# Optimization experiments

Hardware: AMD Instinct MI355X
Metric: run time of the kernel (lower is better)

Reference implementation:

```python
import jax, jax.numpy as jnp
import numpy as np

B, AT, NBR = 8, 96, 512
NG, NT = 25, 5            # n_gaussian_triple, n_theta
NANG = NG * NT            # 125, filternet input dim
NF = 128                  # n_filters
NB = 128                  # n_atom_basis


def ssp(x):
    # shifted softplus: ln(0.5*e^x + 0.5) = softplus(x) - ln(2)
    return jax.nn.softplus(x) - jnp.asarray(np.log(2.0), x.dtype)


def setup_inputs() -> dict:
    key = jax.random.key(0)
    ks = jax.random.split(key, 16)
    s = lambda fan_in: 1.0 / np.sqrt(fan_in)
    return {
        "x": jax.random.normal(ks[0], (B, AT, NB), jnp.float32),
        "triple_ijk": jax.random.uniform(ks[1], (B, AT, NBR, NANG), jnp.float32),
        "neighbors_j": jax.random.randint(ks[2], (B, AT, NBR), 0, AT, jnp.int32),
        "neighbors_k": jax.random.randint(ks[3], (B, AT, NBR), 0, AT, jnp.int32),
        "triple_mask": jnp.ones((B, AT, NBR), jnp.float32),
        # filter network (Dense ssp -> Dense linear)
        "W1": jax.random.normal(ks[4], (NANG, NF), jnp.float32) * s(NANG),
        "b1": jnp.zeros((NF,), jnp.float32),
        "W2": jax.random.normal(ks[5], (NF, NF), jnp.float32) * s(NF),
        "b2": jnp.zeros((NF,), jnp.float32),
        # cfconv in2f (no bias) and f2out (ssp activation)
        "Win": jax.random.normal(ks[6], (NB, NF), jnp.float32) * s(NB),
        "Wf2": jax.random.normal(ks[7], (NF, NB), jnp.float32) * s(NF),
        "bf2": jnp.zeros((NB,), jnp.float32),
        # final dense (linear) before residual
        "Wd": jax.random.normal(ks[8], (NB, NB), jnp.float32) * s(NB),
        "bd": jnp.zeros((NB,), jnp.float32),
    }


def _gather_atoms(y, nbh):
    # y: (B, At, F); nbh: (B, At, Nbr) -> (B, At, Nbr, F)
    b, at, nbr = nbh.shape
    idx = nbh.reshape(b, at * nbr, 1)
    return jnp.take_along_axis(y, idx, axis=1).reshape(b, at, nbr, y.shape[-1])


def reference(x, triple_ijk, neighbors_j, neighbors_k, triple_mask,
              W1, b1, W2, b2, Win, Wf2, bf2, Wd, bd):
    # filter network on angular/radial triple features -> (B, At, Nbr, NF)
    W_triple = ssp(triple_ijk @ W1 + b1) @ W2 + b2
    # in2f
    y = x @ Win                                  # (B, At, NF)
    y_j = _gather_atoms(y, neighbors_j)          # (B, At, Nbr, NF)
    y_k = _gather_atoms(y, neighbors_k)          # (B, At, Nbr, NF)
    # element-wise continuous-filter conv over triples, mask padded triples
    yt = y_j * y_k * W_triple * triple_mask[..., None]
    agg = jnp.sum(yt, axis=2)                    # sum-aggregate over triples
    v = ssp(agg @ Wf2 + bf2)                     # f2out with shifted softplus
    v = v @ Wd + bd                              # interaction dense
    return x + v                                 # residual
```

## Files before the change

### kernel.cpp

```cpp
#include <hip/hip_runtime.h>
#include <math.h>

#define B_    8
#define AT_   96
#define NBR_  512
#define NANG_ 125
#define NF_   128
#define NB_   128
#define TN    32
#define NCHUNK 8
#define CROWS (NBR_ / NCHUNK)
#define TSTRIDE 136

typedef __attribute__((ext_vector_type(8))) short bf16x8;
typedef __attribute__((ext_vector_type(4))) float f32x4;
typedef float f32x4u __attribute__((ext_vector_type(4), aligned(4)));
typedef __attribute__((ext_vector_type(4))) unsigned int u32x4;

__device__ __forceinline__ short f2bf(float f) {
    union { float f; unsigned u; } x; x.f = f;
    return (short)((x.u + 0x8000u) >> 16);
}
__device__ __forceinline__ float bf2f(unsigned short h) {
    union { unsigned u; float f; } x; x.u = ((unsigned)h) << 16;
    return x.f;
}
__device__ __forceinline__ unsigned pk2bf(float a, float b) {
    union { float f; unsigned u; } x, y; x.f = a; y.f = b;
    return ((x.u + 0x8000u) >> 16) | ((y.u + 0x8000u) & 0xffff0000u);
}

__device__ __forceinline__ float sspf(float x) {
    float p = __builtin_amdgcn_exp2f(x * 1.44269504088896340736f);
    float l = __builtin_amdgcn_logf(1.0f + p);
    return 0.69314718055994530942f * l - 0.69314718055994530942f;
}

__global__ __launch_bounds__(128) void prep_kernel(
    const float* __restrict__ x, const float* __restrict__ Win,
    const float* __restrict__ W1, const float* __restrict__ W2,
    float* __restrict__ y, short* __restrict__ w1p, short* __restrict__ w2p)
{
    __shared__ float xs[4][NB_];
    int blk = blockIdx.x, tid = threadIdx.x;
    if (blk < 192) {
        int row0 = blk * 4;
        #pragma unroll
        for (int r = 0; r < 4; r++) xs[r][tid] = x[(row0 + r) * NB_ + tid];
        __syncthreads();
        float a0 = 0.f, a1 = 0.f, a2 = 0.f, a3 = 0.f;
        #pragma unroll 8
        for (int k = 0; k < NB_; k++) {
            float w = Win[k * NF_ + tid];
            a0 = fmaf(xs[0][k], w, a0);
            a1 = fmaf(xs[1][k], w, a1);
            a2 = fmaf(xs[2][k], w, a2);
            a3 = fmaf(xs[3][k], w, a3);
        }
        y[(row0 + 0) * NF_ + tid] = a0;
        y[(row0 + 1) * NF_ + tid] = a1;
        y[(row0 + 2) * NF_ + tid] = a2;
        y[(row0 + 3) * NF_ + tid] = a3;
    } else {
        int t = (blk - 192) * 128 + tid;
        int j = t & 7, lane = (t >> 3) & 63, ks = (t >> 9) & 3, ct = t >> 11;
        int k = ks * 32 + (lane >> 4) * 8 + j;
        int n = ct * 16 + (lane & 15);
        w1p[t] = (k < NANG_) ? f2bf(W1[k * NF_ + n]) : (short)0;
        w2p[t] = f2bf(W2[k * NF_ + n]);
    }
}

__global__ __launch_bounds__(256) void triple_partial(
    const float* __restrict__ trip,
    const int* __restrict__ nbj, const int* __restrict__ nbk,
    const float* __restrict__ maskg,
    const float* __restrict__ b1g, const float* __restrict__ b2g,
    const float* __restrict__ y, const short* __restrict__ w1p,
    const short* __restrict__ w2p, float* __restrict__ pagg)
{
    __shared__ short ts[TN * TSTRIDE];
    __shared__ short hs[TN * TSTRIDE];
    __shared__ unsigned short yjkb[TN * TSTRIDE];

    const int tid = threadIdx.x;
    const int wave = tid >> 6, lane = tid & 63;
    const int quad = lane >> 4, col = lane & 15;
    const int blk = blockIdx.x;
    const int bid = blk >> 3, c = blk & 7;
    const int b = bid / AT_;

    const float* tpc = trip + (long)bid * NBR_ * NANG_ + (long)c * CROWS * NANG_;
    const int nb_base = bid * NBR_ + c * CROWS;

    const int ct0 = 2 * wave, ct1 = 2 * wave + 1;
    const int f0 = ct0 * 16 + col, f1 = ct1 * 16 + col;
    const float bias1_0 = b1g[f0], bias1_1 = b1g[f1];
    const float bias2_0 = b2g[f0], bias2_1 = b2g[f1];

    const int srow = tid >> 3, schunk = tid & 7;

    bf16x8 w1f0[4], w1f1[4], w2f0[4], w2f1[4];
    #pragma unroll
    for (int ks = 0; ks < 4; ks++) {
        w1f0[ks] = *(const bf16x8*)&w1p[(ct0 * 4 + ks) * 512 + lane * 8];
        w1f1[ks] = *(const bf16x8*)&w1p[(ct1 * 4 + ks) * 512 + lane * 8];
        w2f0[ks] = *(const bf16x8*)&w2p[(ct0 * 4 + ks) * 512 + lane * 8];
        w2f1[ks] = *(const bf16x8*)&w2p[(ct1 * 4 + ks) * 512 + lane * 8];
    }

    float accw0 = 0.f, accw1 = 0.f;

    for (int nt = 0; nt < CROWS / TN; nt++) {
        const float* tp = tpc + nt * TN * NANG_;
        const int nrow0 = nb_base + nt * TN;

        const float* rowp = tp + srow * NANG_ + schunk * 16;
        f32x4u v0, v1, v2, v3;
        if (schunk < 7) {
            v0 = *(const f32x4u*)(rowp + 0);
            v1 = *(const f32x4u*)(rowp + 4);
            v2 = *(const f32x4u*)(rowp + 8);
            v3 = *(const f32x4u*)(rowp + 12);
        } else {
            v0 = *(const f32x4u*)(rowp + 0);
            v1 = *(const f32x4u*)(rowp + 4);
            v2 = *(const f32x4u*)(rowp + 8);
            v3.x = rowp[12]; v3.y = 0.f; v3.z = 0.f; v3.w = 0.f;
        }

        const int jj = nbj[nrow0 + srow], kk = nbk[nrow0 + srow];
        const float m = maskg[nrow0 + srow];
        const float* yjp = y + (b * AT_ + jj) * NF_ + schunk * 16;
        const float* ykp = y + (b * AT_ + kk) * NF_ + schunk * 16;
        f32x4 j0 = ((const f32x4*)yjp)[0], j1 = ((const f32x4*)yjp)[1];
        f32x4 j2 = ((const f32x4*)yjp)[2], j3 = ((const f32x4*)yjp)[3];
        f32x4 k0 = ((const f32x4*)ykp)[0], k1 = ((const f32x4*)ykp)[1];
        f32x4 k2 = ((const f32x4*)ykp)[2], k3 = ((const f32x4*)ykp)[3];

        __syncthreads();

        {
            u32x4 pA, pB;
            pA.x = pk2bf(v0.x, v0.y); pA.y = pk2bf(v0.z, v0.w);
            pA.z = pk2bf(v1.x, v1.y); pA.w = pk2bf(v1.z, v1.w);
            pB.x = pk2bf(v2.x, v2.y); pB.y = pk2bf(v2.z, v2.w);
            pB.z = pk2bf(v3.x, v3.y); pB.w = pk2bf(v3.z, v3.w);
            u32x4* dst = (u32x4*)&ts[srow * TSTRIDE + schunk * 16];
            dst[0] = pA;
            dst[1] = pB;
        }
        {
            f32x4 p0 = j0 * k0 * m, p1 = j1 * k1 * m;
            f32x4 p2 = j2 * k2 * m, p3 = j3 * k3 * m;
            u32x4 qA, qB;
            qA.x = pk2bf(p0.x, p0.y); qA.y = pk2bf(p0.z, p0.w);
            qA.z = pk2bf(p1.x, p1.y); qA.w = pk2bf(p1.z, p1.w);
            qB.x = pk2bf(p2.x, p2.y); qB.y = pk2bf(p2.z, p2.w);
            qB.z = pk2bf(p3.x, p3.y); qB.w = pk2bf(p3.z, p3.w);
            u32x4* dst = (u32x4*)&yjkb[srow * TSTRIDE + schunk * 16];
            dst[0] = qA;
            dst[1] = qB;
        }
        __syncthreads();

        f32x4 d00 = {0,0,0,0}, d01 = {0,0,0,0}, d10 = {0,0,0,0}, d11 = {0,0,0,0};
        #pragma unroll
        for (int ks = 0; ks < 4; ks++) {
            bf16x8 a0 = *(const bf16x8*)&ts[(     col) * TSTRIDE + ks * 32 + quad * 8];
            bf16x8 a1 = *(const bf16x8*)&ts[(16 + col) * TSTRIDE + ks * 32 + quad * 8];
            d00 = __builtin_amdgcn_mfma_f32_16x16x32_bf16(a0, w1f0[ks], d00, 0, 0, 0);
            d01 = __builtin_amdgcn_mfma_f32_16x16x32_bf16(a0, w1f1[ks], d01, 0, 0, 0);
            d10 = __builtin_amdgcn_mfma_f32_16x16x32_bf16(a1, w1f0[ks], d10, 0, 0, 0);
            d11 = __builtin_amdgcn_mfma_f32_16x16x32_bf16(a1, w1f1[ks], d11, 0, 0, 0);
        }
        #pragma unroll
        for (int r = 0; r < 4; r++) {
            int row0 = quad * 4 + r, row1 = 16 + quad * 4 + r;
            hs[row0 * TSTRIDE + f0] = f2bf(sspf(d00[r] + bias1_0));
            hs[row0 * TSTRIDE + f1] = f2bf(sspf(d01[r] + bias1_1));
            hs[row1 * TSTRIDE + f0] = f2bf(sspf(d10[r] + bias1_0));
            hs[row1 * TSTRIDE + f1] = f2bf(sspf(d11[r] + bias1_1));
        }
        __syncthreads();

        f32x4 e00 = {0,0,0,0}, e01 = {0,0,0,0}, e10 = {0,0,0,0}, e11 = {0,0,0,0};
        #pragma unroll
        for (int ks = 0; ks < 4; ks++) {
            bf16x8 a0 = *(const bf16x8*)&hs[(     col) * TSTRIDE + ks * 32 + quad * 8];
            bf16x8 a1 = *(const bf16x8*)&hs[(16 + col) * TSTRIDE + ks * 32 + quad * 8];
            e00 = __builtin_amdgcn_mfma_f32_16x16x32_bf16(a0, w2f0[ks], e00, 0, 0, 0);
            e01 = __builtin_amdgcn_mfma_f32_16x16x32_bf16(a0, w2f1[ks], e01, 0, 0, 0);
            e10 = __builtin_amdgcn_mfma_f32_16x16x32_bf16(a1, w2f0[ks], e10, 0, 0, 0);
            e11 = __builtin_amdgcn_mfma_f32_16x16x32_bf16(a1, w2f1[ks], e11, 0, 0, 0);
        }
        #pragma unroll
        for (int r = 0; r < 4; r++) {
            int row0 = quad * 4 + r, row1 = 16 + quad * 4 + r;
            accw0 += (e00[r] + bias2_0) * bf2f(yjkb[row0 * TSTRIDE + f0]);
            accw1 += (e01[r] + bias2_1) * bf2f(yjkb[row0 * TSTRIDE + f1]);
            accw0 += (e10[r] + bias2_0) * bf2f(yjkb[row1 * TSTRIDE + f0]);
            accw1 += (e11[r] + bias2_1) * bf2f(yjkb[row1 * TSTRIDE + f1]);
        }
    }

    accw0 += __shfl_xor(accw0, 16, 64);
    accw0 += __shfl_xor(accw0, 32, 64);
    accw1 += __shfl_xor(accw1, 16, 64);
    accw1 += __shfl_xor(accw1, 32, 64);
    if (quad == 0) {
        pagg[blk * NF_ + f0] = accw0;
        pagg[blk * NF_ + f1] = accw1;
    }
}

__global__ __launch_bounds__(128) void finish_kernel(
    const float* __restrict__ x, const float* __restrict__ pagg,
    const float* __restrict__ Wf2, const float* __restrict__ bf2,
    const float* __restrict__ Wd, const float* __restrict__ bd,
    float* __restrict__ out)
{
    __shared__ float aggs[NF_];
    __shared__ float t1s[NF_];
    int bid = blockIdx.x, f = threadIdx.x;
    float a = 0.f;
    #pragma unroll
    for (int c = 0; c < NCHUNK; c++) a += pagg[(bid * NCHUNK + c) * NF_ + f];
    aggs[f] = a;
    __syncthreads();
    float acc = 0.f;
    #pragma unroll 8
    for (int k = 0; k < NF_; k++) acc = fmaf(aggs[k], Wf2[k * NB_ + f], acc);
    t1s[f] = sspf(acc + bf2[f]);
    __syncthreads();
    acc = 0.f;
    #pragma unroll 8
    for (int k = 0; k < NB_; k++) acc = fmaf(t1s[k], Wd[k * NB_ + f], acc);
    out[bid * NB_ + f] = x[bid * NB_ + f] + acc + bd[f];
}

extern "C" void kernel_launch(void* const* d_in, const int* in_sizes, int n_in,
                              void* d_out, int out_size, void* d_ws, size_t ws_size,
                              hipStream_t stream) {
    const float* x    = (const float*)d_in[0];
    const float* trip = (const float*)d_in[1];
    const int*   nbj  = (const int*)d_in[2];
    const int*   nbk  = (const int*)d_in[3];
    const float* mask = (const float*)d_in[4];
    const float* W1   = (const float*)d_in[5];
    const float* b1   = (const float*)d_in[6];
    const float* W2   = (const float*)d_in[7];
    const float* b2   = (const float*)d_in[8];
    const float* Win  = (const float*)d_in[9];
    const float* Wf2  = (const float*)d_in[10];
    const float* bf2  = (const float*)d_in[11];
    const float* Wd   = (const float*)d_in[12];
    const float* bd   = (const float*)d_in[13];
    float* out = (float*)d_out;

    char* ws = (char*)d_ws;
    float* y    = (float*)ws;
    short* w1p  = (short*)(ws + 393216);
    short* w2p  = (short*)(ws + 393216 + 32768);
    float* pagg = (float*)(ws + 393216 + 65536);

    prep_kernel<<<320, 128, 0, stream>>>(x, Win, W1, W2, y, w1p, w2p);
    triple_partial<<<B_ * AT_ * NCHUNK, 256, 0, stream>>>(trip, nbj, nbk, mask,
        b1, b2, y, w1p, w2p, pagg);
    finish_kernel<<<B_ * AT_, 128, 0, stream>>>(x, pagg, Wf2, bf2, Wd, bd, out);
}
```

Baseline: 347.3 us.

## Double-buffer triple tiles with prefetch and halve chunk count per atom

Result: slower. 366.6 us (+5.5%).

```diff
diff --git a/kernel.cpp b/kernel.cpp
--- a/kernel.cpp
+++ b/kernel.cpp
@@ -8,7 +8,7 @@
 #define NF_   128
 #define NB_   128
 #define TN    32
-#define NCHUNK 8
+#define NCHUNK 4
 #define CROWS (NBR_ / NCHUNK)
 #define TSTRIDE 136
 
@@ -79,15 +79,15 @@
     const float* __restrict__ y, const short* __restrict__ w1p,
     const short* __restrict__ w2p, float* __restrict__ pagg)
 {
-    __shared__ short ts[TN * TSTRIDE];
-    __shared__ short hs[TN * TSTRIDE];
-    __shared__ unsigned short yjkb[TN * TSTRIDE];
+    __shared__ short ts[2][TN * TSTRIDE];
+    __shared__ short hs[2][TN * TSTRIDE];
+    __shared__ unsigned short yjkb[2][TN * TSTRIDE];
 
     const int tid = threadIdx.x;
     const int wave = tid >> 6, lane = tid & 63;
     const int quad = lane >> 4, col = lane & 15;
     const int blk = blockIdx.x;
-    const int bid = blk >> 3, c = blk & 7;
+    const int bid = blk >> 2, c = blk & 3;
     const int b = bid / AT_;
 
     const float* tpc = trip + (long)bid * NBR_ * NANG_ + (long)c * CROWS * NANG_;
@@ -100,75 +100,78 @@
 
     const int srow = tid >> 3, schunk = tid & 7;
 
-    bf16x8 w1f0[4], w1f1[4], w2f0[4], w2f1[4];
+    bf16x8 w1f0[4], w1f1[4];
     #pragma unroll
     for (int ks = 0; ks < 4; ks++) {
         w1f0[ks] = *(const bf16x8*)&w1p[(ct0 * 4 + ks) * 512 + lane * 8];
         w1f1[ks] = *(const bf16x8*)&w1p[(ct1 * 4 + ks) * 512 + lane * 8];
-        w2f0[ks] = *(const bf16x8*)&w2p[(ct0 * 4 + ks) * 512 + lane * 8];
-        w2f1[ks] = *(const bf16x8*)&w2p[(ct1 * 4 + ks) * 512 + lane * 8];
-    }
+    }
+
+    f32x4u tc[2][4];
+
+#define LOAD_TRIP(slot, tile) do {                                          \
+    const float* rowp = tpc + (tile) * TN * NANG_ + srow * NANG_ + schunk * 16; \
+    if (schunk < 7) {                                                       \
+        tc[slot][0] = *(const f32x4u*)(rowp + 0);                           \
+        tc[slot][1] = *(const f32x4u*)(rowp + 4);                           \
+        tc[slot][2] = *(const f32x4u*)(rowp + 8);                           \
+        tc[slot][3] = *(const f32x4u*)(rowp + 12);                          \
+    } else {                                                                \
+        tc[slot][0] = *(const f32x4u*)(rowp + 0);                           \
+        tc[slot][1] = *(const f32x4u*)(rowp + 4);                           \
+        tc[slot][2] = *(const f32x4u*)(rowp + 8);                           \
+        tc[slot][3].x = rowp[12]; tc[slot][3].y = 0.f;                      \
+        tc[slot][3].z = 0.f; tc[slot][3].w = 0.f;                           \
+    } } while (0)
+
+#define STAGE(buf, slot, tile) do {                                         \
+    const int nr = nb_base + (tile) * TN + srow;                            \
+    const int jj = nbj[nr], kk = nbk[nr];                                   \
+    const float m = maskg[nr];                                              \
+    const float* yjp = y + (b * AT_ + jj) * NF_ + schunk * 16;              \
+    const float* ykp = y + (b * AT_ + kk) * NF_ + schunk * 16;              \
+    f32x4 j0 = ((const f32x4*)yjp)[0], j1 = ((const f32x4*)yjp)[1];         \
+    f32x4 j2 = ((const f32x4*)yjp)[2], j3 = ((const f32x4*)yjp)[3];         \
+    f32x4 k0 = ((const f32x4*)ykp)[0], k1 = ((const f32x4*)ykp)[1];         \
+    f32x4 k2 = ((const f32x4*)ykp)[2], k3 = ((const f32x4*)ykp)[3];         \
+    u32x4 pA, pB;                                                           \
+    pA.x = pk2bf(tc[slot][0].x, tc[slot][0].y);                             \
+    pA.y = pk2bf(tc[slot][0].z, tc[slot][0].w);                             \
+    pA.z = pk2bf(tc[slot][1].x, tc[slot][1].y);                             \
+    pA.w = pk2bf(tc[slot][1].z, tc[slot][1].w);                             \
+    pB.x = pk2bf(tc[slot][2].x, tc[slot][2].y);                             \
+    pB.y = pk2bf(tc[slot][2].z, tc[slot][2].w);                             \
+    pB.z = pk2bf(tc[slot][3].x, tc[slot][3].y);                             \
+    pB.w = pk2bf(tc[slot][3].z, tc[slot][3].w);                             \
+    u32x4* dstT = (u32x4*)&ts[buf][srow * TSTRIDE + schunk * 16];           \
+    dstT[0] = pA; dstT[1] = pB;                                             \
+    f32x4 p0 = j0 * k0 * m, p1 = j1 * k1 * m;                               \
+    f32x4 p2 = j2 * k2 * m, p3 = j3 * k3 * m;                               \
+    u32x4 qA, qB;                                                           \
+    qA.x = pk2bf(p0.x, p0.y); qA.y = pk2bf(p0.z, p0.w);                     \
+    qA.z = pk2bf(p1.x, p1.y); qA.w = pk2bf(p1.z, p1.w);                     \
+    qB.x = pk2bf(p2.x, p2.y); qB.y = pk2bf(p2.z, p2.w);                     \
+    qB.z = pk2bf(p3.x, p3.y); qB.w = pk2bf(p3.z, p3.w);                     \
+    u32x4* dstY = (u32x4*)&yjkb[buf][srow * TSTRIDE + schunk * 16];         \
+    dstY[0] = qA; dstY[1] = qB;                                             \
+    } while (0)
 
     float accw0 = 0.f, accw1 = 0.f;
 
-    for (int nt = 0; nt < CROWS / TN; nt++) {
-        const float* tp = tpc + nt * TN * NANG_;
-        const int nrow0 = nb_base + nt * TN;
-
-        const float* rowp = tp + srow * NANG_ + schunk * 16;
-        f32x4u v0, v1, v2, v3;
-        if (schunk < 7) {
-            v0 = *(const f32x4u*)(rowp + 0);
-            v1 = *(const f32x4u*)(rowp + 4);
-            v2 = *(const f32x4u*)(rowp + 8);
-            v3 = *(const f32x4u*)(rowp + 12);
-        } else {
-            v0 = *(const f32x4u*)(rowp + 0);
-            v1 = *(const f32x4u*)(rowp + 4);
-            v2 = *(const f32x4u*)(rowp + 8);
-            v3.x = rowp[12]; v3.y = 0.f; v3.z = 0.f; v3.w = 0.f;
-        }
-
-        const int jj = nbj[nrow0 + srow], kk = nbk[nrow0 + srow];
-        const float m = maskg[nrow0 + srow];
-        const float* yjp = y + (b * AT_ + jj) * NF_ + schunk * 16;
-        const float* ykp = y + (b * AT_ + kk) * NF_ + schunk * 16;
-        f32x4 j0 = ((const f32x4*)yjp)[0], j1 = ((const f32x4*)yjp)[1];
-        f32x4 j2 = ((const f32x4*)yjp)[2], j3 = ((const f32x4*)yjp)[3];
-        f32x4 k0 = ((const f32x4*)ykp)[0], k1 = ((const f32x4*)ykp)[1];
-        f32x4 k2 = ((const f32x4*)ykp)[2], k3 = ((const f32x4*)ykp)[3];
-
-        __syncthreads();
-
-        {
-            u32x4 pA, pB;
-            pA.x = pk2bf(v0.x, v0.y); pA.y = pk2bf(v0.z, v0.w);
-            pA.z = pk2bf(v1.x, v1.y); pA.w = pk2bf(v1.z, v1.w);
-            pB.x = pk2bf(v2.x, v2.y); pB.y = pk2bf(v2.z, v2.w);
-            pB.z = pk2bf(v3.x, v3.y); pB.w = pk2bf(v3.z, v3.w);
-            u32x4* dst = (u32x4*)&ts[srow * TSTRIDE + schunk * 16];
-            dst[0] = pA;
-            dst[1] = pB;
-        }
-        {
-            f32x4 p0 = j0 * k0 * m, p1 = j1 * k1 * m;
-            f32x4 p2 = j2 * k2 * m, p3 = j3 * k3 * m;
-            u32x4 qA, qB;
-            qA.x = pk2bf(p0.x, p0.y); qA.y = pk2bf(p0.z, p0.w);
-            qA.z = pk2bf(p1.x, p1.y); qA.w = pk2bf(p1.z, p1.w);
-            qB.x = pk2bf(p2.x, p2.y); qB.y = pk2bf(p2.z, p2.w);
-            qB.z = pk2bf(p3.x, p3.y); qB.w = pk2bf(p3.z, p3.w);
-            u32x4* dst = (u32x4*)&yjkb[srow * TSTRIDE + schunk * 16];
-            dst[0] = qA;
-            dst[1] = qB;
-        }
-        __syncthreads();
+    LOAD_TRIP(0, 0);
+    LOAD_TRIP(1, 1);
+    STAGE(0, 0, 0);
+    __syncthreads();
+
+    #pragma unroll
+    for (int nt = 0; nt < 4; nt++) {
+        const int p = nt & 1;
 
         f32x4 d00 = {0,0,0,0}, d01 = {0,0,0,0}, d10 = {0,0,0,0}, d11 = {0,0,0,0};
         #pragma unroll
         for (int ks = 0; ks < 4; ks++) {
-            bf16x8 a0 = *(const bf16x8*)&ts[(     col) * TSTRIDE + ks * 32 + quad * 8];
-            bf16x8 a1 = *(const bf16x8*)&ts[(16 + col) * TSTRIDE + ks * 32 + quad * 8];
+            bf16x8 a0 = *(const bf16x8*)&ts[p][(     col) * TSTRIDE + ks * 32 + quad * 8];
+            bf16x8 a1 = *(const bf16x8*)&ts[p][(16 + col) * TSTRIDE + ks * 32 + quad * 8];
             d00 = __builtin_amdgcn_mfma_f32_16x16x32_bf16(a0, w1f0[ks], d00, 0, 0, 0);
             d01 = __builtin_amdgcn_mfma_f32_16x16x32_bf16(a0, w1f1[ks], d01, 0, 0, 0);
             d10 = __builtin_amdgcn_mfma_f32_16x16x32_bf16(a1, w1f0[ks], d10, 0, 0, 0);
@@ -177,18 +180,29 @@
         #pragma unroll
         for (int r = 0; r < 4; r++) {
             int row0 = quad * 4 + r, row1 = 16 + quad * 4 + r;
-            hs[row0 * TSTRIDE + f0] = f2bf(sspf(d00[r] + bias1_0));
-            hs[row0 * TSTRIDE + f1] = f2bf(sspf(d01[r] + bias1_1));
-            hs[row1 * TSTRIDE + f0] = f2bf(sspf(d10[r] + bias1_0));
-            hs[row1 * TSTRIDE + f1] = f2bf(sspf(d11[r] + bias1_1));
+            hs[p][row0 * TSTRIDE + f0] = f2bf(sspf(d00[r] + bias1_0));
+            hs[p][row0 * TSTRIDE + f1] = f2bf(sspf(d01[r] + bias1_1));
+            hs[p][row1 * TSTRIDE + f0] = f2bf(sspf(d10[r] + bias1_0));
+            hs[p][row1 * TSTRIDE + f1] = f2bf(sspf(d11[r] + bias1_1));
         }
         __syncthreads();
 
+        if (nt < 2) LOAD_TRIP(p, nt + 2);
+
+        bf16x8 w2f0[4], w2f1[4];
+        #pragma unroll
+        for (int ks = 0; ks < 4; ks++) {
+            w2f0[ks] = *(const bf16x8*)&w2p[(ct0 * 4 + ks) * 512 + lane * 8];
+            w2f1[ks] = *(const bf16x8*)&w2p[(ct1 * 4 + ks) * 512 + lane * 8];
+        }
+
+        if (nt < 3) STAGE(p ^ 1, p ^ 1, nt + 1);
+
         f32x4 e00 = {0,0,0,0}, e01 = {0,0,0,0}, e10 = {0,0,0,0}, e11 = {0,0,0,0};
         #pragma unroll
         for (int ks = 0; ks < 4; ks++) {
-            bf16x8 a0 = *(const bf16x8*)&hs[(     col) * TSTRIDE + ks * 32 + quad * 8];
-            bf16x8 a1 = *(const bf16x8*)&hs[(16 + col) * TSTRIDE + ks * 32 + quad * 8];
+            bf16x8 a0 = *(const bf16x8*)&hs[p][(     col) * TSTRIDE + ks * 32 + quad * 8];
+            bf16x8 a1 = *(const bf16x8*)&hs[p][(16 + col) * TSTRIDE + ks * 32 + quad * 8];
             e00 = __builtin_amdgcn_mfma_f32_16x16x32_bf16(a0, w2f0[ks], e00, 0, 0, 0);
             e01 = __builtin_amdgcn_mfma_f32_16x16x32_bf16(a0, w2f1[ks], e01, 0, 0, 0);
             e10 = __builtin_amdgcn_mfma_f32_16x16x32_bf16(a1, w2f0[ks], e10, 0, 0, 0);
@@ -197,12 +211,16 @@
         #pragma unroll
         for (int r = 0; r < 4; r++) {
             int row0 = quad * 4 + r, row1 = 16 + quad * 4 + r;
-            accw0 += (e00[r] + bias2_0) * bf2f(yjkb[row0 * TSTRIDE + f0]);
-            accw1 += (e01[r] + bias2_1) * bf2f(yjkb[row0 * TSTRIDE + f1]);
-            accw0 += (e10[r] + bias2_0) * bf2f(yjkb[row1 * TSTRIDE + f0]);
-            accw1 += (e11[r] + bias2_1) * bf2f(yjkb[row1 * TSTRIDE + f1]);
-        }
-    }
+            accw0 += (e00[r] + bias2_0) * bf2f(yjkb[p][row0 * TSTRIDE + f0]);
+            accw1 += (e01[r] + bias2_1) * bf2f(yjkb[p][row0 * TSTRIDE + f1]);
+            accw0 += (e10[r] + bias2_0) * bf2f(yjkb[p][row1 * TSTRIDE + f0]);
+            accw1 += (e11[r] + bias2_1) * bf2f(yjkb[p][row1 * TSTRIDE + f1]);
+        }
+
+        if (nt < 3) __syncthreads();
+    }
+#undef LOAD_TRIP
+#undef STAGE
 
     accw0 += __shfl_xor(accw0, 16, 64);
     accw0 += __shfl_xor(accw0, 32, 64);
```

## Load triple features straight into MFMA A-fragments, dropping LDS staging

Applied to the files above, without the earlier changes.

New measurement: 393.4 us. +13.3%, slower.

```diff
diff --git a/kernel.cpp b/kernel.cpp
--- a/kernel.cpp
+++ b/kernel.cpp
@@ -79,7 +79,6 @@
     const float* __restrict__ y, const short* __restrict__ w1p,
     const short* __restrict__ w2p, float* __restrict__ pagg)
 {
-    __shared__ short ts[TN * TSTRIDE];
     __shared__ short hs[TN * TSTRIDE];
     __shared__ unsigned short yjkb[TN * TSTRIDE];
 
@@ -100,57 +99,29 @@
 
     const int srow = tid >> 3, schunk = tid & 7;
 
-    bf16x8 w1f0[4], w1f1[4], w2f0[4], w2f1[4];
+    bf16x8 w1f0[4], w1f1[4];
     #pragma unroll
     for (int ks = 0; ks < 4; ks++) {
         w1f0[ks] = *(const bf16x8*)&w1p[(ct0 * 4 + ks) * 512 + lane * 8];
         w1f1[ks] = *(const bf16x8*)&w1p[(ct1 * 4 + ks) * 512 + lane * 8];
-        w2f0[ks] = *(const bf16x8*)&w2p[(ct0 * 4 + ks) * 512 + lane * 8];
-        w2f1[ks] = *(const bf16x8*)&w2p[(ct1 * 4 + ks) * 512 + lane * 8];
     }
 
     float accw0 = 0.f, accw1 = 0.f;
 
+    #pragma unroll
     for (int nt = 0; nt < CROWS / TN; nt++) {
         const float* tp = tpc + nt * TN * NANG_;
-        const int nrow0 = nb_base + nt * TN;
-
-        const float* rowp = tp + srow * NANG_ + schunk * 16;
-        f32x4u v0, v1, v2, v3;
-        if (schunk < 7) {
-            v0 = *(const f32x4u*)(rowp + 0);
-            v1 = *(const f32x4u*)(rowp + 4);
-            v2 = *(const f32x4u*)(rowp + 8);
-            v3 = *(const f32x4u*)(rowp + 12);
-        } else {
-            v0 = *(const f32x4u*)(rowp + 0);
-            v1 = *(const f32x4u*)(rowp + 4);
-            v2 = *(const f32x4u*)(rowp + 8);
-            v3.x = rowp[12]; v3.y = 0.f; v3.z = 0.f; v3.w = 0.f;
-        }
-
-        const int jj = nbj[nrow0 + srow], kk = nbk[nrow0 + srow];
-        const float m = maskg[nrow0 + srow];
-        const float* yjp = y + (b * AT_ + jj) * NF_ + schunk * 16;
-        const float* ykp = y + (b * AT_ + kk) * NF_ + schunk * 16;
-        f32x4 j0 = ((const f32x4*)yjp)[0], j1 = ((const f32x4*)yjp)[1];
-        f32x4 j2 = ((const f32x4*)yjp)[2], j3 = ((const f32x4*)yjp)[3];
-        f32x4 k0 = ((const f32x4*)ykp)[0], k1 = ((const f32x4*)ykp)[1];
-        f32x4 k2 = ((const f32x4*)ykp)[2], k3 = ((const f32x4*)ykp)[3];
-
-        __syncthreads();
 
         {
-            u32x4 pA, pB;
-            pA.x = pk2bf(v0.x, v0.y); pA.y = pk2bf(v0.z, v0.w);
-            pA.z = pk2bf(v1.x, v1.y); pA.w = pk2bf(v1.z, v1.w);
-            pB.x = pk2bf(v2.x, v2.y); pB.y = pk2bf(v2.z, v2.w);
-            pB.z = pk2bf(v3.x, v3.y); pB.w = pk2bf(v3.z, v3.w);
-            u32x4* dst = (u32x4*)&ts[srow * TSTRIDE + schunk * 16];
-            dst[0] = pA;
-            dst[1] = pB;
-        }
-        {
+            const int nr = nb_base + nt * TN + srow;
+            const int jj = nbj[nr], kk = nbk[nr];
+            const float m = maskg[nr];
+            const float* yjp = y + (b * AT_ + jj) * NF_ + schunk * 16;
+            const float* ykp = y + (b * AT_ + kk) * NF_ + schunk * 16;
+            f32x4 j0 = ((const f32x4*)yjp)[0], j1 = ((const f32x4*)yjp)[1];
+            f32x4 j2 = ((const f32x4*)yjp)[2], j3 = ((const f32x4*)yjp)[3];
+            f32x4 k0 = ((const f32x4*)ykp)[0], k1 = ((const f32x4*)ykp)[1];
+            f32x4 k2 = ((const f32x4*)ykp)[2], k3 = ((const f32x4*)ykp)[3];
             f32x4 p0 = j0 * k0 * m, p1 = j1 * k1 * m;
             f32x4 p2 = j2 * k2 * m, p3 = j3 * k3 * m;
             u32x4 qA, qB;
@@ -162,17 +133,38 @@
             dst[0] = qA;
             dst[1] = qB;
         }
-        __syncthreads();
+
+        bf16x8 a0f[4], a1f[4];
+        #pragma unroll
+        for (int ks = 0; ks < 4; ks++) {
+            const float* r0 = tp + col * NANG_ + ks * 32 + quad * 8;
+            const float* r1 = tp + (16 + col) * NANG_ + ks * 32 + quad * 8;
+            f32x4u u0a = *(const f32x4u*)r0;
+            f32x4u u0b = *(const f32x4u*)r1;
+            f32x4u u1a, u1b;
+            if (ks == 3 && quad == 3) {
+                u1a.x = r0[4]; u1a.y = 0.f; u1a.z = 0.f; u1a.w = 0.f;
+                u1b.x = r1[4]; u1b.y = 0.f; u1b.z = 0.f; u1b.w = 0.f;
+            } else {
+                u1a = *(const f32x4u*)(r0 + 4);
+                u1b = *(const f32x4u*)(r1 + 4);
+            }
+            union { u32x4 u; bf16x8 v; } pa, pb;
+            pa.u.x = pk2bf(u0a.x, u0a.y); pa.u.y = pk2bf(u0a.z, u0a.w);
+            pa.u.z = pk2bf(u1a.x, u1a.y); pa.u.w = pk2bf(u1a.z, u1a.w);
+            pb.u.x = pk2bf(u0b.x, u0b.y); pb.u.y = pk2bf(u0b.z, u0b.w);
+            pb.u.z = pk2bf(u1b.x, u1b.y); pb.u.w = pk2bf(u1b.z, u1b.w);
+            a0f[ks] = pa.v;
+            a1f[ks] = pb.v;
+        }
 
         f32x4 d00 = {0,0,0,0}, d01 = {0,0,0,0}, d10 = {0,0,0,0}, d11 = {0,0,0,0};
         #pragma unroll
         for (int ks = 0; ks < 4; ks++) {
-            bf16x8 a0 = *(const bf16x8*)&ts[(     col) * TSTRIDE + ks * 32 + quad * 8];
-            bf16x8 a1 = *(const bf16x8*)&ts[(16 + col) * TSTRIDE + ks * 32 + quad * 8];
-            d00 = __builtin_amdgcn_mfma_f32_16x16x32_bf16(a0, w1f0[ks], d00, 0, 0, 0);
-            d01 = __builtin_amdgcn_mfma_f32_16x16x32_bf16(a0, w1f1[ks], d01, 0, 0, 0);
-            d10 = __builtin_amdgcn_mfma_f32_16x16x32_bf16(a1, w1f0[ks], d10, 0, 0, 0);
-            d11 = __builtin_amdgcn_mfma_f32_16x16x32_bf16(a1, w1f1[ks], d11, 0, 0, 0);
+            d00 = __builtin_amdgcn_mfma_f32_16x16x32_bf16(a0f[ks], w1f0[ks], d00, 0, 0, 0);
+            d01 = __builtin_amdgcn_mfma_f32_16x16x32_bf16(a0f[ks], w1f1[ks], d01, 0, 0, 0);
+            d10 = __builtin_amdgcn_mfma_f32_16x16x32_bf16(a1f[ks], w1f0[ks], d10, 0, 0, 0);
+            d11 = __builtin_amdgcn_mfma_f32_16x16x32_bf16(a1f[ks], w1f1[ks], d11, 0, 0, 0);
         }
         #pragma unroll
         for (int r = 0; r < 4; r++) {
@@ -184,15 +176,22 @@
         }
         __syncthreads();
 
+        bf16x8 w2f0[4], w2f1[4];
+        #pragma unroll
+        for (int ks = 0; ks < 4; ks++) {
+            w2f0[ks] = *(const bf16x8*)&w2p[(ct0 * 4 + ks) * 512 + lane * 8];
+            w2f1[ks] = *(const bf16x8*)&w2p[(ct1 * 4 + ks) * 512 + lane * 8];
+        }
+
         f32x4 e00 = {0,0,0,0}, e01 = {0,0,0,0}, e10 = {0,0,0,0}, e11 = {0,0,0,0};
         #pragma unroll
         for (int ks = 0; ks < 4; ks++) {
-            bf16x8 a0 = *(const bf16x8*)&hs[(     col) * TSTRIDE + ks * 32 + quad * 8];
-            bf16x8 a1 = *(const bf16x8*)&hs[(16 + col) * TSTRIDE + ks * 32 + quad * 8];
-            e00 = __builtin_amdgcn_mfma_f32_16x16x32_bf16(a0, w2f0[ks], e00, 0, 0, 0);
-            e01 = __builtin_amdgcn_mfma_f32_16x16x32_bf16(a0, w2f1[ks], e01, 0, 0, 0);
-            e10 = __builtin_amdgcn_mfma_f32_16x16x32_bf16(a1, w2f0[ks], e10, 0, 0, 0);
-            e11 = __builtin_amdgcn_mfma_f32_16x16x32_bf16(a1, w2f1[ks], e11, 0, 0, 0);
+            bf16x8 h0 = *(const bf16x8*)&hs[(     col) * TSTRIDE + ks * 32 + quad * 8];
+            bf16x8 h1 = *(const bf16x8*)&hs[(16 + col) * TSTRIDE + ks * 32 + quad * 8];
+            e00 = __builtin_amdgcn_mfma_f32_16x16x32_bf16(h0, w2f0[ks], e00, 0, 0, 0);
+            e01 = __builtin_amdgcn_mfma_f32_16x16x32_bf16(h0, w2f1[ks], e01, 0, 0, 0);
+            e10 = __builtin_amdgcn_mfma_f32_16x16x32_bf16(h1, w2f0[ks], e10, 0, 0, 0);
+            e11 = __builtin_amdgcn_mfma_f32_16x16x32_bf16(h1, w2f1[ks], e11, 0, 0, 0);
         }
         #pragma unroll
         for (int r = 0; r < 4; r++) {
@@ -202,6 +201,8 @@
             accw0 += (e10[r] + bias2_0) * bf2f(yjkb[row1 * TSTRIDE + f0]);
             accw1 += (e11[r] + bias2_1) * bf2f(yjkb[row1 * TSTRIDE + f1]);
         }
+
+        if (nt + 1 < CROWS / TN) __syncthreads();
     }
 
     accw0 += __shfl_xor(accw0, 16, 64);
```
